# Performance work log

Hardware: AMD Instinct MI355X
Metric: run time of the kernel (lower is better)

The kernel has to match this reference:

```python
import jax, jax.numpy as jnp
import numpy as np

SCALE = 2
K_UP = 5
PAD_UNF = (K_UP // 2) * SCALE  # nn.Unfold padding = k_up//2 * scale = 4
BN_INV = float(1.0 / np.sqrt(1.0 + 1e-5))  # BN inference with running_mean=0, running_var=1


def conv2d(x, w, pad):
    return jax.lax.conv_general_dilated(
        x, w, window_strides=(1, 1), padding=[(pad, pad), (pad, pad)],
        dimension_numbers=('NCHW', 'OIHW', 'NCHW'))


def bn(x, g, b):
    return x * (g * BN_INV)[None, :, None, None] + b[None, :, None, None]


def upsample_bilinear_ac(x, oh, ow):
    # bilinear, align_corners=True
    b, c, h, w = x.shape
    ys = jnp.linspace(0.0, h - 1.0, oh)
    xs = jnp.linspace(0.0, w - 1.0, ow)
    y0 = jnp.floor(ys).astype(jnp.int32)
    x0 = jnp.floor(xs).astype(jnp.int32)
    y1 = jnp.minimum(y0 + 1, h - 1)
    x1 = jnp.minimum(x0 + 1, w - 1)
    wy = (ys - y0)[:, None]  # (oh,1)
    wx = (xs - x0)          # (ow,)
    top = x[:, :, y0, :]
    bot = x[:, :, y1, :]
    top = top[:, :, :, x0] * (1.0 - wx) + top[:, :, :, x1] * wx
    bot = bot[:, :, :, x0] * (1.0 - wx) + bot[:, :, :, x1] * wx
    return top * (1.0 - wy) + bot * wy


def setup_inputs() -> dict:
    key = jax.random.key(0)
    ks = jax.random.split(key, 16)
    B, N, C = 4, 4096, 128  # h=w=64
    CL, CM, OUT = 128, 64, 128
    R = C // 4

    def rn(k, shape, s=0.05):
        return s * jax.random.normal(k, shape, dtype=jnp.float32)

    d = {}
    d['x_h'] = rn(ks[0], (B, N, C), 1.0)
    d['x_l'] = rn(ks[1], (B, N * SCALE * SCALE, CL), 1.0)
    # conv_reduce 3x3 C->C
    d['wr'] = rn(ks[2], (C, C, 3, 3))
    d['wr_g'] = jnp.ones((C,), jnp.float32); d['wr_b'] = jnp.zeros((C,), jnp.float32)
    # conv1 1x1 C->CM
    d['w1'] = rn(ks[3], (CM, C, 1, 1))
    d['w1_g'] = jnp.ones((CM,), jnp.float32); d['w1_b'] = jnp.zeros((CM,), jnp.float32)
    # conv2 1x1 2*CL->CM
    d['w2'] = rn(ks[4], (CM, 2 * CL, 1, 1))
    d['w2_g'] = jnp.ones((CM,), jnp.float32); d['w2_b'] = jnp.zeros((CM,), jnp.float32)
    # enc 3x3 2*CM -> k_up^2
    d['we'] = rn(ks[5], (K_UP * K_UP, 2 * CM, 3, 3))
    d['we_g'] = jnp.ones((K_UP * K_UP,), jnp.float32); d['we_b'] = jnp.zeros((K_UP * K_UP,), jnp.float32)
    # channel attention fc1/fc2 (1x1 convs with bias)
    d['wf1'] = rn(ks[6], (R, C, 1, 1)); d['bf1'] = jnp.zeros((R,), jnp.float32)
    d['wf2'] = rn(ks[7], (C, R, 1, 1)); d['bf2'] = jnp.zeros((C,), jnp.float32)
    # conv_out: 3x3 (C+CL)->OUT, then 1x1 OUT->OUT
    d['wo1'] = rn(ks[8], (OUT, C + CL, 3, 3))
    d['wo1_g'] = jnp.ones((OUT,), jnp.float32); d['wo1_b'] = jnp.zeros((OUT,), jnp.float32)
    d['wo2'] = rn(ks[9], (OUT, OUT, 1, 1))
    d['wo2_g'] = jnp.ones((OUT,), jnp.float32); d['wo2_b'] = jnp.zeros((OUT,), jnp.float32)
    return d


def reference(x_h, x_l, wr, wr_g, wr_b, w1, w1_g, w1_b, w2, w2_g, w2_b,
              we, we_g, we_b, wf1, bf1, wf2, bf2,
              wo1, wo1_g, wo1_b, wo2, wo2_g, wo2_b):
    B, N, C = x_h.shape
    h = int(round(N ** 0.5)); w = h
    h_, w_ = h * SCALE, w * SCALE
    xh = jnp.transpose(x_h, (0, 2, 1)).reshape(B, C, h, w)
    xl = jnp.transpose(x_l, (0, 2, 1)).reshape(B, -1, h_, w_)

    # x1 = upsample(conv1(x_h))
    x1 = upsample_bilinear_ac(jax.nn.relu(bn(conv2d(xh, w1, 0), w1_g, w1_b)), h_, w_)

    # channel attention on x_l
    g_c = jnp.mean(xl, axis=(2, 3), keepdims=True)  # (B,CL,1,1)
    g_c = conv2d(g_c, wf1, 0) + bf1[None, :, None, None]
    g_c = jax.nn.relu(g_c)
    g_c = conv2d(g_c, wf2, 0) + bf2[None, :, None, None]
    g_c = jax.nn.sigmoid(g_c) * xl

    x2 = jax.nn.relu(bn(conv2d(jnp.concatenate((g_c, xl), axis=1), w2, 0), w2_g, w2_b))

    # kernel prediction + softmax over k_up^2
    Wk = bn(conv2d(jnp.concatenate((x1, x2), axis=1), we, 1), we_g, we_b)
    Wk = jax.nn.softmax(Wk, axis=1)  # (B, 25, h_, w_)

    # reduce + upsample high-res feature
    xr = jax.nn.relu(bn(conv2d(xh, wr, 1), wr_g, wr_b))
    xup = upsample_bilinear_ac(xr, h_, w_)  # (B, C, h_, w_)

    # CARAFE-style reassembly: accumulate over k_up^2 dilated offsets
    xp = jnp.pad(xup, ((0, 0), (0, 0), (PAD_UNF, PAD_UNF), (PAD_UNF, PAD_UNF)))
    X = jnp.zeros_like(xup)
    idx = 0
    for i in range(K_UP):
        for j in range(K_UP):
            patch = xp[:, :, i * SCALE:i * SCALE + h_, j * SCALE:j * SCALE + w_]
            X = X + patch * Wk[:, idx][:, None]
            idx += 1

    y = jnp.concatenate((X, xl), axis=1)
    y = jax.nn.relu(bn(conv2d(y, wo1, 1), wo1_g, wo1_b))
    y = jax.nn.relu(bn(conv2d(y, wo2, 0), wo2_g, wo2_b))
    return y
```

## Files before the change

kernel.cpp:

```cpp
#include <hip/hip_runtime.h>
#include <hip/hip_bf16.h>

#define BN_INV 0.99999500003749968f

typedef __attribute__((ext_vector_type(8))) short bf16x8;
typedef __attribute__((ext_vector_type(4))) float f32x4;
typedef __attribute__((ext_vector_type(8))) unsigned short ushort8;
typedef unsigned short u16;

__device__ inline u16 f2bf(float f) {
  union { float f; unsigned int u; } v;
  v.f = f;
  unsigned int r = v.u + 0x7FFFu + ((v.u >> 16) & 1u);
  return (u16)(r >> 16);
}
__device__ inline float bf2f(u16 u) {
  union { unsigned int u; float f; } v;
  v.u = ((unsigned int)u) << 16;
  return v.f;
}
__device__ inline float asf(unsigned int u) {
  union { unsigned int u; float f; } v; v.u = u; return v.f;
}
__device__ inline void unpack8(bf16x8 v, float* f) {
  union { bf16x8 v; unsigned int w[4]; } u; u.v = v;
#pragma unroll
  for (int q = 0; q < 4; ++q) {
    f[2 * q]     = asf(u.w[q] << 16);
    f[2 * q + 1] = asf(u.w[q] & 0xFFFF0000u);
  }
}

#define GLOAD_LDS16(g, l)                                              \
  __builtin_amdgcn_global_load_lds(                                    \
      (const __attribute__((address_space(1))) unsigned int*)(g),      \
      (__attribute__((address_space(3))) unsigned int*)(l), 16, 0, 0)

__global__ __launch_bounds__(256) void k_setup(
    u16* __restrict__ pad, u16* __restrict__ xcat, u16* __restrict__ xhp,
    const float* __restrict__ wr, const float* __restrict__ wrg,
    const float* __restrict__ we, const float* __restrict__ weg,
    const float* __restrict__ wo1, const float* __restrict__ wo1g,
    const float* __restrict__ wo2, const float* __restrict__ wo2g,
    const float* __restrict__ w1, const float* __restrict__ w1g,
    u16* __restrict__ wr_bf, u16* __restrict__ we_bf, u16* __restrict__ wo1bf,
    u16* __restrict__ wo2bf, u16* __restrict__ w1bf) {
  int blk = blockIdx.x;
  if (blk < 56) {
    u16* buf; int PADW, CH, nb, b0;
    if (blk < 32)      { buf = pad;  PADW = 130; CH = 256; nb = 32; b0 = 0; }
    else if (blk < 48) { buf = xcat; PADW = 130; CH = 128; nb = 16; b0 = 32; }
    else               { buf = xhp;  PADW = 66;  CH = 128; nb = 8;  b0 = 48; }
    int nring = 2 * PADW + 2 * (PADW - 2);
    int vecs = CH >> 3;
    int total = 4 * nring * vecs;
    ushort8 z = {0, 0, 0, 0, 0, 0, 0, 0};
    for (int i = (blk - b0) * 256 + threadIdx.x; i < total; i += nb * 256) {
      int v = i % vecs;
      int r = (i / vecs) % nring;
      int b = i / (vecs * nring);
      int y, x;
      if (r < PADW) { y = 0; x = r; }
      else if (r < 2 * PADW) { y = PADW - 1; x = r - PADW; }
      else { int s = r - 2 * PADW; y = 1 + (s >> 1); x = (s & 1) ? (PADW - 1) : 0; }
      *(ushort8*)(buf + ((size_t)(b * PADW + y) * PADW + x) * CH + v * 8) = z;
    }
    return;
  }
  blk -= 56;
  const float *w, *g; u16* out; int Cout, Cin, OPAD, TAPS, base;
  if (blk < 576)       { w = wr;  g = wrg;  out = wr_bf; Cout = 128; Cin = 128; OPAD = 128; TAPS = 9; base = 0; }
  else if (blk < 720)  { w = we;  g = weg;  out = we_bf; Cout = 25;  Cin = 128; OPAD = 32;  TAPS = 9; base = 576; }
  else if (blk < 1872) { w = wo1; g = wo1g; out = wo1bf; Cout = 128; Cin = 256; OPAD = 128; TAPS = 9; base = 720; }
  else if (blk < 1936) { w = wo2; g = wo2g; out = wo2bf; Cout = 128; Cin = 128; OPAD = 128; TAPS = 1; base = 1872; }
  else                 { w = w1;  g = w1g;  out = w1bf;  Cout = 64;  Cin = 128; OPAD = 64;  TAPS = 1; base = 1936; }
  int idx = (blk - base) * 256 + threadIdx.x;
  int c = idx % Cin;
  int o = (idx / Cin) % OPAD;
  int tap = idx / (Cin * OPAD);
  float v = 0.f;
  if (o < Cout) v = w[(o * Cin + c) * TAPS + tap] * g[o] * BN_INV;
  out[idx] = f2bf(v);
}

template <int PADW, int CIN, int NOUT, int NB, int TILE_M, int EPI, int NTHR,
          int WAVES_N>
__global__ __launch_bounds__(NTHR, 1) void k_conv_mfma(
    const u16* __restrict__ pad, const u16* __restrict__ wb,
    const float* __restrict__ bias, void* __restrict__ outp) {
  constexpr int H = PADW - 2;
  constexpr int NSEG = NOUT / NB;
  constexpr int KQ = CIN / 64;
  constexpr int NSTEPS = 9 * KQ;
  constexpr int NWAVES = NTHR / 64;
  constexpr int WAVES_M = NWAVES / WAVES_N;
  constexpr int WN = NB / WAVES_N;
  constexpr int NF = WN / 16;
  constexpr int WM = TILE_M / WAVES_M;
  constexpr int MF = WM / 16;
  constexpr int GRID = 4 * H * NSEG;
  constexpr int CPX = GRID / 8;
  constexpr int ALOADS = TILE_M * 8;
  constexpr int BLOADS = NB * 8;
  __shared__ alignas(16) u16 As[2][TILE_M * 64];
  __shared__ alignas(16) u16 Bs[2][NB * 64];

  int tid = threadIdx.x, wv = tid >> 6, l = tid & 63;
  int wrw = wv / WAVES_N, wc = wv % WAVES_N;
  int bid0 = blockIdx.x;
  int bid = (bid0 & 7) * CPX + (bid0 >> 3);
  int ns = (NSEG > 1) ? (bid % NSEG) : 0;
  int row = (NSEG > 1) ? (bid / NSEG) : bid;
  int b = row / H, y = row % H;
  const u16* pbat = pad + (size_t)b * PADW * PADW * CIN;

  auto stage = [&](int t, int bufi) {
    int tap = t / KQ;
    int ch0 = (t % KQ) * 64;
    int ky = tap / 3, kx = tap % 3;
    const u16* arow = pbat + ((size_t)(y + ky) * PADW + kx) * CIN + ch0;
#pragma unroll
    for (int j = 0; j < ALOADS / NTHR; ++j) {
      int q = j * NTHR + tid;
      int px = q >> 3;
      int sl = (q & 7) ^ (px & 7);
      GLOAD_LDS16(arow + (size_t)px * CIN + sl * 8,
                  (char*)&As[bufi][0] + (size_t)(j * NTHR + (tid & ~63)) * 16);
    }
    const u16* brow = wb + ((size_t)tap * NOUT + ns * NB) * CIN + ch0;
#pragma unroll
    for (int j = 0; j < BLOADS / NTHR; ++j) {
      int q = j * NTHR + tid;
      int co = q >> 3;
      int sl = (q & 7) ^ (co & 7);
      GLOAD_LDS16(brow + (size_t)co * CIN + sl * 8,
                  (char*)&Bs[bufi][0] + (size_t)(j * NTHR + (tid & ~63)) * 16);
    }
    if constexpr (BLOADS % NTHR) {
      if (tid < BLOADS % NTHR) {
        int q = (BLOADS / NTHR) * NTHR + tid;
        int co = q >> 3;
        int sl = (q & 7) ^ (co & 7);
        GLOAD_LDS16(brow + (size_t)co * CIN + sl * 8,
                    (char*)&Bs[bufi][0] +
                        (size_t)((BLOADS / NTHR) * NTHR + (tid & ~63)) * 16);
      }
    }
  };

  f32x4 acc[MF][NF];
#pragma unroll
  for (int m = 0; m < MF; ++m)
#pragma unroll
    for (int n = 0; n < NF; ++n) acc[m][n] = (f32x4){0.f, 0.f, 0.f, 0.f};

  stage(0, 0);
  for (int t = 0; t < NSTEPS; ++t) {
    __syncthreads();
    if (t + 1 < NSTEPS) stage(t + 1, (t + 1) & 1);
    const u16* Ab = &As[t & 1][0];
    const u16* Bb = &Bs[t & 1][0];
    bf16x8 Bf[2][NF];
#pragma unroll
    for (int kf = 0; kf < 2; ++kf)
#pragma unroll
      for (int n = 0; n < NF; ++n) {
        int co = wc * WN + n * 16 + (l & 15);
        int sl = (kf * 4 + (l >> 4)) ^ (co & 7);
        Bf[kf][n] = *(const bf16x8*)((const char*)Bb + co * 128 + sl * 16);
      }
#pragma unroll
    for (int m = 0; m < MF; ++m) {
      int px = wrw * WM + m * 16 + (l & 15);
      int s0 = (l >> 4) ^ (px & 7);
      int s1 = (4 + (l >> 4)) ^ (px & 7);
      bf16x8 a0 = *(const bf16x8*)((const char*)Ab + px * 128 + s0 * 16);
      bf16x8 a1 = *(const bf16x8*)((const char*)Ab + px * 128 + s1 * 16);
#pragma unroll
      for (int n = 0; n < NF; ++n) {
        acc[m][n] = __builtin_amdgcn_mfma_f32_16x16x32_bf16(a0, Bf[0][n], acc[m][n], 0, 0, 0);
        acc[m][n] = __builtin_amdgcn_mfma_f32_16x16x32_bf16(a1, Bf[1][n], acc[m][n], 0, 0, 0);
      }
    }
  }

  int ncol = l & 15, rq = l >> 4;
  size_t pixb = ((size_t)b * H + y) * H;
  if constexpr (EPI == 0) {
    u16* ob = (u16*)outp;
#pragma unroll
    for (int m = 0; m < MF; ++m) {
      int px0 = wrw * WM + m * 16 + rq * 4;
#pragma unroll
      for (int n = 0; n < NF; ++n) {
        int o = ns * NB + wc * WN + n * 16 + ncol;
        float be = bias[o];
#pragma unroll
        for (int r = 0; r < 4; ++r)
          ob[(pixb + px0 + r) * NOUT + o] = f2bf(fmaxf(acc[m][n][r] + be, 0.f));
      }
    }
  } else {
    float* sm = (float*)&As[0][0];
    __syncthreads();
#pragma unroll
    for (int m = 0; m < MF; ++m) {
      int px0 = wrw * WM + m * 16 + rq * 4;
#pragma unroll
      for (int n = 0; n < NF; ++n) {
        int o = wc * WN + n * 16 + ncol;
        float be = (o < 25) ? bias[o] : 0.f;
#pragma unroll
        for (int r = 0; r < 4; ++r)
          sm[(px0 + r) * 33 + o] = acc[m][n][r] + be;
      }
    }
    __syncthreads();
    if (tid < TILE_M) {
      int px = tid;
      float v[25];
      float mx = -1e30f;
#pragma unroll
      for (int i = 0; i < 25; ++i) {
        v[i] = sm[px * 33 + i];
        mx = fmaxf(mx, v[i]);
      }
      float s = 0.f;
#pragma unroll
      for (int i = 0; i < 25; ++i) {
        v[i] = expf(v[i] - mx);
        s += v[i];
      }
      float inv = 1.f / s;
      float* wkp = (float*)outp + (pixb + px) * 25;
#pragma unroll
      for (int i = 0; i < 25; ++i) wkp[i] = v[i] * inv;
    }
  }
}

__global__ __launch_bounds__(256) void k_stage_in(
    const float* __restrict__ xh, const float* __restrict__ xl,
    u16* __restrict__ xhp, u16* __restrict__ pad, float* __restrict__ gpart) {
  int blk = blockIdx.x;
  int tid = threadIdx.x;
  if (blk < 1024) {
    int idx = blk * 256 + tid;
    int c0 = (idx & 15) * 8;
    int p = idx >> 4;
    int b = p >> 12, pp = p & 4095;
    int y = pp >> 6, x = pp & 63;
    const float* s = xh + (size_t)p * 128 + c0;
    ushort8 o;
#pragma unroll
    for (int j = 0; j < 8; ++j) o[j] = f2bf(s[j]);
    *(ushort8*)(xhp + ((size_t)(b * 66 + y + 1) * 66 + (x + 1)) * 128 + c0) = o;
    return;
  }
  int blk2 = blk - 1024;
  int c0 = (tid & 15) * 8;
  int pxl = tid >> 4;
  int b = (blk2 * 64) >> 14;
  float facc[8] = {0.f, 0.f, 0.f, 0.f, 0.f, 0.f, 0.f, 0.f};
#pragma unroll
  for (int it = 0; it < 4; ++it) {
    int p = blk2 * 64 + it * 16 + pxl;
    int pp = p & 16383;
    int y = pp >> 7, x = pp & 127;
    const float* s = xl + (size_t)p * 128 + c0;
    ushort8 o;
#pragma unroll
    for (int j = 0; j < 8; ++j) {
      float f = s[j];
      facc[j] += f;
      o[j] = f2bf(f);
    }
    *(ushort8*)(pad + ((size_t)(b * 130 + y + 1) * 130 + (x + 1)) * 256 + 128 + c0) = o;
  }
  __shared__ float red[16][16][9];
#pragma unroll
  for (int j = 0; j < 8; ++j) red[pxl][tid & 15][j] = facc[j];
  __syncthreads();
  if (tid < 128) {
    float sum = 0.f;
#pragma unroll
    for (int q = 0; q < 16; ++q) sum += red[q][tid >> 3][tid & 7];
    atomicAdd(&gpart[(size_t)(blk2 & 63) * 512 + b * 128 + tid], sum);
  }
}

__global__ __launch_bounds__(128) void k_semlp(
    const float* __restrict__ gpart, const float* __restrict__ wf1,
    const float* __restrict__ bf1, const float* __restrict__ wf2,
    const float* __restrict__ bf2, const float* __restrict__ w2,
    const float* __restrict__ w2g, u16* __restrict__ weffb) {
  int b = blockIdx.x;
  int t = threadIdx.x;
  __shared__ float m[128], hid[32], sg[128];
  float s0 = 0.f;
  for (int s = 0; s < 64; ++s) s0 += gpart[(size_t)s * 512 + b * 128 + t];
  m[t] = s0 * (1.0f / 16384.0f);
  __syncthreads();
  if (t < 32) {
    float a = 0.f;
    for (int c = 0; c < 128; ++c) a += wf1[t * 128 + c] * m[c];
    hid[t] = fmaxf(a + bf1[t], 0.f);
  }
  __syncthreads();
  {
    float a = 0.f;
    for (int r = 0; r < 32; ++r) a += wf2[t * 32 + r] * hid[r];
    a += bf2[t];
    sg[t] = 1.f / (1.f + expf(-a));
  }
  __syncthreads();
  for (int o = 0; o < 64; ++o) {
    float sc = w2g[o] * BN_INV;
    weffb[((size_t)b * 64 + o) * 128 + t] =
        f2bf((w2[o * 256 + t] * sg[t] + w2[o * 256 + 128 + t]) * sc);
  }
}

__global__ __launch_bounds__(256) void k_t1x2(
    const u16* __restrict__ xhp, const u16* __restrict__ w1b,
    const float* __restrict__ w1bias, u16* __restrict__ t1b,
    const u16* __restrict__ pad, const u16* __restrict__ weffb,
    const float* __restrict__ x2bias, u16* __restrict__ xcat_pad) {
  int t = threadIdx.x;
  int wv = t >> 6, l = t & 63;
  int kg = l >> 4;
  if (blockIdx.x < 256) {
    int blk = blockIdx.x;
    int b = blk >> 6, y = blk & 63;
    int m0 = wv * 16;
    int xc = m0 + (l & 15);
    const u16* abase = xhp + ((size_t)(b * 66 + y + 1) * 66 + xc + 1) * 128 + kg * 8;
    const u16* bbase = w1b + (size_t)(l & 15) * 128 + kg * 8;
    f32x4 acc[4];
#pragma unroll
    for (int i = 0; i < 4; ++i) acc[i] = (f32x4){0.f, 0.f, 0.f, 0.f};
#pragma unroll
    for (int cc = 0; cc < 4; ++cc) {
      bf16x8 a = *(const bf16x8*)(abase + cc * 32);
#pragma unroll
      for (int nf = 0; nf < 4; ++nf) {
        bf16x8 bfr = *(const bf16x8*)(bbase + nf * 16 * 128 + cc * 32);
        acc[nf] = __builtin_amdgcn_mfma_f32_16x16x32_bf16(a, bfr, acc[nf], 0, 0, 0);
      }
    }
    int prow = m0 + (l >> 4) * 4;
    int ncol = l & 15;
    size_t pixb = ((size_t)b << 12) + ((size_t)y << 6);
#pragma unroll
    for (int nf = 0; nf < 4; ++nf) {
      int o = nf * 16 + ncol;
      float be = w1bias[o];
#pragma unroll
      for (int r = 0; r < 4; ++r)
        t1b[(pixb + prow + r) * 64 + o] = f2bf(fmaxf(acc[nf][r] + be, 0.f));
    }
    return;
  }
  int blk = blockIdx.x - 256;
  int b = blk >> 8, rr = blk & 255;
  int y = rr >> 1;
  int xseg = (rr & 1) << 6;
  int m0 = xseg + wv * 16;
  int xc = m0 + (l & 15);
  const u16* abase =
      pad + ((size_t)(b * 130 + y + 1) * 130 + xc + 1) * 256 + 128 + kg * 8;
  const u16* bbase = weffb + (size_t)b * 64 * 128 + (size_t)(l & 15) * 128 + kg * 8;
  f32x4 acc[4];
#pragma unroll
  for (int i = 0; i < 4; ++i) acc[i] = (f32x4){0.f, 0.f, 0.f, 0.f};
#pragma unroll
  for (int cc = 0; cc < 4; ++cc) {
    bf16x8 a = *(const bf16x8*)(abase + cc * 32);
#pragma unroll
    for (int nf = 0; nf < 4; ++nf) {
      bf16x8 bfr = *(const bf16x8*)(bbase + nf * 16 * 128 + cc * 32);
      acc[nf] = __builtin_amdgcn_mfma_f32_16x16x32_bf16(a, bfr, acc[nf], 0, 0, 0);
    }
  }
  int prow = m0 + (l >> 4) * 4;
  int ncol = l & 15;
  size_t rb = (size_t)(b * 130 + y + 1) * 130;
#pragma unroll
  for (int nf = 0; nf < 4; ++nf) {
    int o = nf * 16 + ncol;
    float be = x2bias[o];
#pragma unroll
    for (int r = 0; r < 4; ++r)
      xcat_pad[(rb + prow + r + 1) * 128 + 64 + o] =
          f2bf(fmaxf(acc[nf][r] + be, 0.f));
  }
}

__global__ __launch_bounds__(256) void k_up64_pad(const u16* __restrict__ in,
                                                  u16* __restrict__ pad) {
  int t = threadIdx.x;
  int c0 = (t & 7) * 8;
  int px = t >> 3;
  int g = blockIdx.x * 32 + px;
  int b = g >> 14, pp = g & 16383;
  int oy = pp >> 7, ox = pp & 127;
  const float S = 63.0f / 127.0f;
  float fy = oy * S, fx = ox * S;
  int y0 = (int)fy, x0 = (int)fx;
  int y1 = min(y0 + 1, 63), x1 = min(x0 + 1, 63);
  float wy = fy - y0, wx = fx - x0;
  const u16* base = in + (size_t)b * 4096 * 64 + c0;
  bf16x8 v00 = *(const bf16x8*)(base + ((y0 << 6) + x0) * 64);
  bf16x8 v01 = *(const bf16x8*)(base + ((y0 << 6) + x1) * 64);
  bf16x8 v10 = *(const bf16x8*)(base + ((y1 << 6) + x0) * 64);
  bf16x8 v11 = *(const bf16x8*)(base + ((y1 << 6) + x1) * 64);
  float f00[8], f01[8], f10[8], f11[8];
  unpack8(v00, f00); unpack8(v01, f01); unpack8(v10, f10); unpack8(v11, f11);
  ushort8 o;
#pragma unroll
  for (int j = 0; j < 8; ++j) {
    float top = f00[j] * (1.f - wx) + f01[j] * wx;
    float bot = f10[j] * (1.f - wx) + f11[j] * wx;
    o[j] = f2bf(top * (1.f - wy) + bot * wy);
  }
  *(ushort8*)(pad + ((size_t)(b * 130 + oy + 1) * 130 + ox + 1) * 128 + c0) = o;
}

__global__ __launch_bounds__(256) void k_up128_bf(
    const u16* __restrict__ in, u16* __restrict__ outb) {
  int t = threadIdx.x;
  int c0 = (t & 15) * 8;
  int px = t >> 4;
  int g = blockIdx.x * 16 + px;
  int b = g >> 14, pp = g & 16383;
  int oy = pp >> 7, ox = pp & 127;
  const float S = 63.0f / 127.0f;
  float fy = oy * S, fx = ox * S;
  int y0 = (int)fy, x0 = (int)fx;
  int y1 = min(y0 + 1, 63), x1 = min(x0 + 1, 63);
  float wy = fy - y0, wx = fx - x0;
  const u16* base = in + (size_t)b * 4096 * 128 + c0;
  bf16x8 v00 = *(const bf16x8*)(base + ((y0 << 6) + x0) * 128);
  bf16x8 v01 = *(const bf16x8*)(base + ((y0 << 6) + x1) * 128);
  bf16x8 v10 = *(const bf16x8*)(base + ((y1 << 6) + x0) * 128);
  bf16x8 v11 = *(const bf16x8*)(base + ((y1 << 6) + x1) * 128);
  float f00[8], f01[8], f10[8], f11[8];
  unpack8(v00, f00); unpack8(v01, f01); unpack8(v10, f10); unpack8(v11, f11);
  ushort8 o;
#pragma unroll
  for (int j = 0; j < 8; ++j) {
    float top = f00[j] * (1.f - wx) + f01[j] * wx;
    float bot = f10[j] * (1.f - wx) + f11[j] * wx;
    o[j] = f2bf(top * (1.f - wy) + bot * wy);
  }
  *(ushort8*)(outb + (size_t)g * 128 + c0) = o;
}

__global__ __launch_bounds__(256) void k_carafe_bf(
    const u16* __restrict__ xup, const float* __restrict__ wk,
    u16* __restrict__ pad) {
  int t = threadIdx.x;
  int c0 = (t & 15) * 8;
  int px = t >> 4;
  int blk = (blockIdx.x & 7) * 512 + (blockIdx.x >> 3);
  int g = blk * 16 + px;
  int b = g >> 14, pp = g & 16383;
  int y = pp >> 7, x = pp & 127;
  __shared__ float wl[16][26];
  for (int i = t; i < 400; i += 256)
    wl[i / 25][i % 25] = wk[(size_t)(blk * 16 + i / 25) * 25 + (i % 25)];
  __syncthreads();
  float acc[8] = {0.f, 0.f, 0.f, 0.f, 0.f, 0.f, 0.f, 0.f};
  const u16* base = xup + ((size_t)b << 14) * 128 + c0;
#pragma unroll
  for (int i = 0; i < 5; ++i) {
    int row = y + 2 * i - 4;
    if ((unsigned)row >= 128u) continue;
#pragma unroll
    for (int jj = 0; jj < 5; ++jj) {
      int col = x + 2 * jj - 4;
      if ((unsigned)col >= 128u) continue;
      bf16x8 v = *(const bf16x8*)(base + (size_t)((row << 7) + col) * 128);
      float w = wl[px][i * 5 + jj];
      float f[8];
      unpack8(v, f);
#pragma unroll
      for (int k = 0; k < 8; ++k) acc[k] += w * f[k];
    }
  }
  ushort8 o;
#pragma unroll
  for (int k = 0; k < 8; ++k) o[k] = f2bf(acc[k]);
  *(ushort8*)(pad + ((size_t)(b * 130 + y + 1) * 130 + (x + 1)) * 256 + c0) = o;
}

__global__ __launch_bounds__(256) void k_wo2_mfma(
    const u16* __restrict__ y1, const u16* __restrict__ wb,
    const float* __restrict__ bb, float* __restrict__ out) {
  int t = threadIdx.x;
  int wv = t >> 6, l = t & 63;
  int blk = blockIdx.x;
  int b = blk >> 8, rr = blk & 255;
  int y = rr >> 1;
  int xseg = (rr & 1) << 6;
  int m0 = xseg + wv * 16;
  int xc = m0 + (l & 15);
  int kg = l >> 4;
  const u16* abase =
      y1 + ((size_t)((b << 14) + (y << 7) + xc)) * 128 + kg * 8;
  const u16* bbase = wb + (size_t)(l & 15) * 128 + kg * 8;
  f32x4 acc[8];
#pragma unroll
  for (int i = 0; i < 8; ++i) acc[i] = (f32x4){0.f, 0.f, 0.f, 0.f};
#pragma unroll
  for (int cc = 0; cc < 4; ++cc) {
    bf16x8 a = *(const bf16x8*)(abase + cc * 32);
#pragma unroll
    for (int nf = 0; nf < 8; ++nf) {
      bf16x8 bfr = *(const bf16x8*)(bbase + nf * 16 * 128 + cc * 32);
      acc[nf] = __builtin_amdgcn_mfma_f32_16x16x32_bf16(a, bfr, acc[nf], 0, 0, 0);
    }
  }
  __shared__ float lds[128 * 65];
  int lpx0 = wv * 16 + (l >> 4) * 4;
  int ncol = l & 15;
#pragma unroll
  for (int nf = 0; nf < 8; ++nf) {
    int o = nf * 16 + ncol;
    float be = bb[o];
#pragma unroll
    for (int r = 0; r < 4; ++r)
      lds[o * 65 + lpx0 + r] = fmaxf(acc[nf][r] + be, 0.f);
  }
  __syncthreads();
  size_t obase = (((size_t)(b * 128)) * 128 + y) * 128 + xseg;
#pragma unroll
  for (int rep = 0; rep < 8; ++rep) {
    int idx = rep * 256 + t;
    int o = idx >> 4;
    int x4 = (idx & 15) * 4;
    f32x4 v;
#pragma unroll
    for (int k = 0; k < 4; ++k) v[k] = lds[o * 65 + x4 + k];
    *(f32x4*)(out + obase + (size_t)o * 16384 + x4) = v;
  }
}

extern "C" void kernel_launch(void* const* d_in, const int* in_sizes, int n_in,
                              void* d_out, int out_size, void* d_ws,
                              size_t ws_size, hipStream_t stream) {
  const float* x_h  = (const float*)d_in[0];
  const float* x_l  = (const float*)d_in[1];
  const float* wr   = (const float*)d_in[2];
  const float* wr_g = (const float*)d_in[3];
  const float* wr_b = (const float*)d_in[4];
  const float* w1   = (const float*)d_in[5];
  const float* w1_g = (const float*)d_in[6];
  const float* w1_b = (const float*)d_in[7];
  const float* w2   = (const float*)d_in[8];
  const float* w2_g = (const float*)d_in[9];
  const float* w2_b = (const float*)d_in[10];
  const float* we   = (const float*)d_in[11];
  const float* we_g = (const float*)d_in[12];
  const float* we_b = (const float*)d_in[13];
  const float* wf1  = (const float*)d_in[14];
  const float* bf1  = (const float*)d_in[15];
  const float* wf2  = (const float*)d_in[16];
  const float* bf2  = (const float*)d_in[17];
  const float* wo1  = (const float*)d_in[18];
  const float* wo1_g= (const float*)d_in[19];
  const float* wo1_b= (const float*)d_in[20];
  const float* wo2  = (const float*)d_in[21];
  const float* wo2_g= (const float*)d_in[22];
  const float* wo2_b= (const float*)d_in[23];
  float* out = (float*)d_out;

  float* ws = (float*)d_ws;
  u16* pad      = (u16*)ws;
  u16* xcat_pad = (u16*)(ws + 8652800);
  u16* xup      = xcat_pad;
  float* wkb   = ws + 12979200;
  u16* t1b = (u16*)(ws + 14617600);
  u16* xr  = (u16*)(ws + 14617600);
  float* y1reg = ws + 15666176;
  u16* y1     = (u16*)y1reg;
  u16* xh_pad = (u16*)y1reg;
  float* gpart = ws + 19860480;
  u16* weff_bf = (u16*)(gpart + 32768);
  float* tail  = gpart + 32768 + 16384;
  u16* wr_bf = (u16*)tail;
  u16* we_bf = (u16*)(tail + 73728);
  u16* wo1bf = (u16*)(tail + 73728 + 18432);
  u16* wo2bf = (u16*)(tail + 73728 + 18432 + 147456);
  u16* w1bf  = (u16*)(tail + 73728 + 18432 + 147456 + 8192);

  hipMemsetAsync(gpart, 0, 32768 * sizeof(float), stream);
  k_setup<<<2024, 256, 0, stream>>>(pad, xcat_pad, xh_pad,
                                    wr, wr_g, we, we_g, wo1, wo1_g,
                                    wo2, wo2_g, w1, w1_g,
                                    wr_bf, we_bf, wo1bf, wo2bf, w1bf);

  k_stage_in<<<2048, 256, 0, stream>>>(x_h, x_l, xh_pad, pad, gpart);
  k_semlp<<<4, 128, 0, stream>>>(gpart, wf1, bf1, wf2, bf2, w2, w2_g, weff_bf);
  k_t1x2<<<1280, 256, 0, stream>>>(xh_pad, w1bf, w1_b, t1b,
                                   pad, weff_bf, w2_b, xcat_pad);
  k_up64_pad<<<2048, 256, 0, stream>>>(t1b, xcat_pad);

  k_conv_mfma<130, 128, 32, 32, 128, 2, 512, 2><<<512, 512, 0, stream>>>(
      xcat_pad, we_bf, we_b, wkb);
  k_conv_mfma<66, 128, 128, 64, 64, 0, 512, 4><<<512, 512, 0, stream>>>(
      xh_pad, wr_bf, wr_b, xr);
  k_up128_bf<<<4096, 256, 0, stream>>>(xr, xup);
  k_carafe_bf<<<4096, 256, 0, stream>>>(xup, wkb, pad);
  k_conv_mfma<130, 256, 128, 128, 128, 0, 512, 4><<<512, 512, 0, stream>>>(
      pad, wo1bf, wo1_b, y1);
  k_wo2_mfma<<<1024, 256, 0, stream>>>(y1, wo2bf, wo2_b, out);
}
```

Before: 185.1 us.

## Fuse 3x3 wo1 conv with 1x1 wo2 conv in one kernel

Replaces the templated wo1 3x3 conv and the separate wo2 1x1 kernel with a single kernel that computes a 128-pixel row of wo1 output, keeps it as bf16 in swizzled LDS, then applies the wo2 1x1 MFMA GEMM and writes NCHW output directly. This removes the y1 intermediate global write and read plus one launch. The fused kernel uses its own double-buffered direct-to-LDS staging and a specialised tile shape, which may schedule differently from the previous templated conv, and it runs one 512-thread block per CU under launch bounds.

```diff
diff --git a/kernel.cpp b/kernel.cpp
--- a/kernel.cpp
+++ b/kernel.cpp
@@ -239,6 +239,133 @@
   }
 }
 
+__global__ __launch_bounds__(512, 1) void k_wo1wo2(
+    const u16* __restrict__ pad, const u16* __restrict__ wb,
+    const float* __restrict__ bias, const u16* __restrict__ w2b,
+    const float* __restrict__ bias2, float* __restrict__ out) {
+  constexpr int PADW = 130, CIN = 256, NOUT = 128, TILE_M = 128;
+  constexpr int H = 128, KQ = 4, NSTEPS = 36;
+  constexpr int WN = 32, NF = 2, WM = 64, MF = 4;
+  __shared__ alignas(16) u16 smem[32768];
+
+  int tid = threadIdx.x, wv = tid >> 6, l = tid & 63;
+  int wrw = wv >> 2, wc = wv & 3;
+  int bid0 = blockIdx.x;
+  int bid = (bid0 & 7) * 64 + (bid0 >> 3);
+  int b = bid >> 7, y = bid & 127;
+  const u16* pbat = pad + (size_t)b * PADW * PADW * CIN;
+
+  auto stage = [&](int t, int bufi) {
+    int tap = t / KQ;
+    int ch0 = (t % KQ) * 64;
+    int ky = tap / 3, kx = tap % 3;
+    const u16* arow = pbat + ((size_t)(y + ky) * PADW + kx) * CIN + ch0;
+#pragma unroll
+    for (int j = 0; j < 2; ++j) {
+      int q = j * 512 + tid;
+      int px = q >> 3;
+      int sl = (q & 7) ^ (px & 7);
+      GLOAD_LDS16(arow + (size_t)px * CIN + sl * 8,
+                  (char*)smem + (size_t)bufi * 16384 +
+                      (size_t)(j * 512 + (tid & ~63)) * 16);
+    }
+    const u16* brow = wb + (size_t)tap * NOUT * CIN + ch0;
+#pragma unroll
+    for (int j = 0; j < 2; ++j) {
+      int q = j * 512 + tid;
+      int co = q >> 3;
+      int sl = (q & 7) ^ (co & 7);
+      GLOAD_LDS16(brow + (size_t)co * CIN + sl * 8,
+                  (char*)smem + 32768 + (size_t)bufi * 16384 +
+                      (size_t)(j * 512 + (tid & ~63)) * 16);
+    }
+  };
+
+  f32x4 acc[MF][NF];
+#pragma unroll
+  for (int m = 0; m < MF; ++m)
+#pragma unroll
+    for (int n = 0; n < NF; ++n) acc[m][n] = (f32x4){0.f, 0.f, 0.f, 0.f};
+
+  stage(0, 0);
+  for (int t = 0; t < NSTEPS; ++t) {
+    __syncthreads();
+    if (t + 1 < NSTEPS) stage(t + 1, (t + 1) & 1);
+    const u16* Ab = smem + (size_t)(t & 1) * 8192;
+    const u16* Bb = smem + 16384 + (size_t)(t & 1) * 8192;
+    bf16x8 Bf[2][NF];
+#pragma unroll
+    for (int kf = 0; kf < 2; ++kf)
+#pragma unroll
+      for (int n = 0; n < NF; ++n) {
+        int co = wc * WN + n * 16 + (l & 15);
+        int sl = (kf * 4 + (l >> 4)) ^ (co & 7);
+        Bf[kf][n] = *(const bf16x8*)((const char*)Bb + co * 128 + sl * 16);
+      }
+#pragma unroll
+    for (int m = 0; m < MF; ++m) {
+      int px = wrw * WM + m * 16 + (l & 15);
+      int s0 = (l >> 4) ^ (px & 7);
+      int s1 = (4 + (l >> 4)) ^ (px & 7);
+      bf16x8 a0 = *(const bf16x8*)((const char*)Ab + px * 128 + s0 * 16);
+      bf16x8 a1 = *(const bf16x8*)((const char*)Ab + px * 128 + s1 * 16);
+#pragma unroll
+      for (int n = 0; n < NF; ++n) {
+        acc[m][n] = __builtin_amdgcn_mfma_f32_16x16x32_bf16(a0, Bf[0][n], acc[m][n], 0, 0, 0);
+        acc[m][n] = __builtin_amdgcn_mfma_f32_16x16x32_bf16(a1, Bf[1][n], acc[m][n], 0, 0, 0);
+      }
+    }
+  }
+
+  __syncthreads();
+  u16* y1t = smem;
+  int ncol = l & 15, rq = l >> 4;
+#pragma unroll
+  for (int m = 0; m < MF; ++m) {
+    int px0 = wrw * WM + m * 16 + rq * 4;
+#pragma unroll
+    for (int n = 0; n < NF; ++n) {
+      int ch = wc * WN + n * 16 + ncol;
+      float be = bias[ch];
+#pragma unroll
+      for (int r = 0; r < 4; ++r) {
+        int px = px0 + r;
+        int g = (ch >> 3) ^ (px & 7);
+        y1t[px * 128 + g * 8 + (ch & 7)] =
+            f2bf(fmaxf(acc[m][n][r] + be, 0.f));
+      }
+    }
+  }
+  __syncthreads();
+
+  f32x4 acc2[8];
+#pragma unroll
+  for (int i = 0; i < 8; ++i) acc2[i] = (f32x4){0.f, 0.f, 0.f, 0.f};
+  int kg = l >> 4;
+  int pxa = wv * 16 + (l & 15);
+  const u16* bbase = w2b + (size_t)(l & 15) * 128 + kg * 8;
+#pragma unroll
+  for (int cc = 0; cc < 4; ++cc) {
+    int g = (kg + cc * 4) ^ (pxa & 7);
+    bf16x8 a = *(const bf16x8*)(y1t + pxa * 128 + g * 8);
+#pragma unroll
+    for (int nf = 0; nf < 8; ++nf) {
+      bf16x8 bfr = *(const bf16x8*)(bbase + nf * 16 * 128 + cc * 32);
+      acc2[nf] = __builtin_amdgcn_mfma_f32_16x16x32_bf16(a, bfr, acc2[nf], 0, 0, 0);
+    }
+  }
+  size_t obase = ((size_t)b * 128) * 16384 + (size_t)y * 128 + wv * 16 + rq * 4;
+#pragma unroll
+  for (int nf = 0; nf < 8; ++nf) {
+    int o = nf * 16 + ncol;
+    float be2 = bias2[o];
+    f32x4 rv;
+#pragma unroll
+    for (int k2 = 0; k2 < 4; ++k2) rv[k2] = fmaxf(acc2[nf][k2] + be2, 0.f);
+    *(f32x4*)(out + obase + (size_t)o * 16384) = rv;
+  }
+}
+
 __global__ __launch_bounds__(256) void k_stage_in(
     const float* __restrict__ xh, const float* __restrict__ xl,
     u16* __restrict__ xhp, u16* __restrict__ pad, float* __restrict__ gpart) {
@@ -492,58 +619,6 @@
 #pragma unroll
   for (int k = 0; k < 8; ++k) o[k] = f2bf(acc[k]);
   *(ushort8*)(pad + ((size_t)(b * 130 + y + 1) * 130 + (x + 1)) * 256 + c0) = o;
-}
-
-__global__ __launch_bounds__(256) void k_wo2_mfma(
-    const u16* __restrict__ y1, const u16* __restrict__ wb,
-    const float* __restrict__ bb, float* __restrict__ out) {
-  int t = threadIdx.x;
-  int wv = t >> 6, l = t & 63;
-  int blk = blockIdx.x;
-  int b = blk >> 8, rr = blk & 255;
-  int y = rr >> 1;
-  int xseg = (rr & 1) << 6;
-  int m0 = xseg + wv * 16;
-  int xc = m0 + (l & 15);
-  int kg = l >> 4;
-  const u16* abase =
-      y1 + ((size_t)((b << 14) + (y << 7) + xc)) * 128 + kg * 8;
-  const u16* bbase = wb + (size_t)(l & 15) * 128 + kg * 8;
-  f32x4 acc[8];
-#pragma unroll
-  for (int i = 0; i < 8; ++i) acc[i] = (f32x4){0.f, 0.f, 0.f, 0.f};
-#pragma unroll
-  for (int cc = 0; cc < 4; ++cc) {
-    bf16x8 a = *(const bf16x8*)(abase + cc * 32);
-#pragma unroll
-    for (int nf = 0; nf < 8; ++nf) {
-      bf16x8 bfr = *(const bf16x8*)(bbase + nf * 16 * 128 + cc * 32);
-      acc[nf] = __builtin_amdgcn_mfma_f32_16x16x32_bf16(a, bfr, acc[nf], 0, 0, 0);
-    }
-  }
-  __shared__ float lds[128 * 65];
-  int lpx0 = wv * 16 + (l >> 4) * 4;
-  int ncol = l & 15;
-#pragma unroll
-  for (int nf = 0; nf < 8; ++nf) {
-    int o = nf * 16 + ncol;
-    float be = bb[o];
-#pragma unroll
-    for (int r = 0; r < 4; ++r)
-      lds[o * 65 + lpx0 + r] = fmaxf(acc[nf][r] + be, 0.f);
-  }
-  __syncthreads();
-  size_t obase = (((size_t)(b * 128)) * 128 + y) * 128 + xseg;
-#pragma unroll
-  for (int rep = 0; rep < 8; ++rep) {
-    int idx = rep * 256 + t;
-    int o = idx >> 4;
-    int x4 = (idx & 15) * 4;
-    f32x4 v;
-#pragma unroll
-    for (int k = 0; k < 4; ++k) v[k] = lds[o * 65 + x4 + k];
-    *(f32x4*)(out + obase + (size_t)o * 16384 + x4) = v;
-  }
 }
 
 extern "C" void kernel_launch(void* const* d_in, const int* in_sizes, int n_in,
@@ -583,7 +658,6 @@
   u16* t1b = (u16*)(ws + 14617600);
   u16* xr  = (u16*)(ws + 14617600);
   float* y1reg = ws + 15666176;
-  u16* y1     = (u16*)y1reg;
   u16* xh_pad = (u16*)y1reg;
   float* gpart = ws + 19860480;
   u16* weff_bf = (u16*)(gpart + 32768);
@@ -612,7 +686,5 @@
       xh_pad, wr_bf, wr_b, xr);
   k_up128_bf<<<4096, 256, 0, stream>>>(xr, xup);
   k_carafe_bf<<<4096, 256, 0, stream>>>(xup, wkb, pad);
-  k_conv_mfma<130, 256, 128, 128, 128, 0, 512, 4><<<512, 512, 0, stream>>>(
-      pad, wo1bf, wo1_b, y1);
-  k_wo2_mfma<<<1024, 256, 0, stream>>>(y1, wo2bf, wo2_b, out);
-}
+  k_wo1wo2<<<512, 512, 0, stream>>>(pad, wo1bf, wo1_b, wo2bf, wo2_b, out);
+}
```

Measured after the change: 176.1 us, median of 2. 4.9% less time.
